# Kernel tuning notes

Measured on AMD Instinct MI355X. Metric: run time of the kernel, lower is better.

## Reference

```python
import jax, jax.numpy as jnp
import numpy as np

N, D, H = 100000, 128, 128
NB, NA, NP, NI = 120000, 200000, 250000, 30000


def _mlp(x, w1, b1, w2, b2):
    # small 2-layer readout MLP: Linear -> ReLU -> Linear
    return jnp.maximum(x @ w1 + b1, 0.0) @ w2 + b2


def _symmetry_pool(node_reps, idx, perms, w1, b1, w2, b2):
    # gather node reps by interaction indices, concat per permutation,
    # apply readout MLP, sum over symmetry permutations
    out = None
    for perm in perms:
        rep = jnp.concatenate([node_reps[idx[:, i]] for i in perm], axis=1)
        y = _mlp(rep, w1, b1, w2, b2)
        out = y if out is None else out + y
    return out


def setup_inputs() -> dict:
    key = jax.random.key(0)
    ks = jax.random.split(key, 32)
    inp = {
        'node_reps': jax.random.normal(ks[0], (N, D), dtype=jnp.float32),
        'bond_idx': jax.random.randint(ks[1], (NB, 2), 0, N),
        'angle_idx': jax.random.randint(ks[2], (NA, 3), 0, N),
        'proper_idx': jax.random.randint(ks[3], (NP, 4), 0, N),
        'improper_idx': jax.random.randint(ks[4], (NI, 4), 0, N),
    }
    # readout MLP params: (in_dim, out_dim) per term
    dims = {'a': (D, 2), 'b': (2 * D, 2), 'g': (3 * D, 2), 'p': (4 * D, 6), 'i': (4 * D, 6)}
    ki = 5
    for tag, (din, dout) in dims.items():
        inp[f'{tag}w1'] = jax.random.normal(ks[ki], (din, H), dtype=jnp.float32) * 0.05
        inp[f'{tag}b1'] = jnp.zeros((H,), dtype=jnp.float32)
        inp[f'{tag}w2'] = jax.random.normal(ks[ki + 1], (H, dout), dtype=jnp.float32) * 0.05
        inp[f'{tag}b2'] = jnp.zeros((dout,), dtype=jnp.float32)
        ki += 2
    return inp


def reference(node_reps, bond_idx, angle_idx, proper_idx, improper_idx,
              aw1, ab1, aw2, ab2,
              bw1, bb1, bw2, bb2,
              gw1, gb1, gw2, gb2,
              pw1, pb1, pw2, pb2,
              iw1, ib1, iw2, ib2):
    atoms = _mlp(node_reps, aw1, ab1, aw2, ab2)
    bonds = _symmetry_pool(node_reps, bond_idx, [(0, 1), (1, 0)], bw1, bb1, bw2, bb2)
    angles = _symmetry_pool(node_reps, angle_idx, [(0, 1, 2), (2, 1, 0)], gw1, gb1, gw2, gb2)
    propers = _symmetry_pool(node_reps, proper_idx, [(0, 1, 2, 3), (3, 2, 1, 0)], pw1, pb1, pw2, pb2)
    # improper perms: central atom at position 1, cyclic perms of others [0,2,3]
    improper_perms = [(0, 1, 2, 3), (2, 1, 3, 0), (3, 1, 0, 2)]
    impropers = _symmetry_pool(node_reps, improper_idx, improper_perms, iw1, ib1, iw2, ib2)
    return (atoms, bonds, angles, propers, impropers)
```

## Files before the change

### kernel.cpp

```cpp
#include <hip/hip_runtime.h>

#define PBLK 256

typedef __attribute__((ext_vector_type(8))) short bf16x8;
typedef __attribute__((ext_vector_type(16))) float f32x16;

__device__ __forceinline__ unsigned short f2bf(float x) {
    unsigned int u = __builtin_bit_cast(unsigned int, x);
    u += 0x7fffu + ((u >> 16) & 1u);
    return (unsigned short)(u >> 16);
}

__global__ void conv_node(const float* __restrict__ x, unsigned short* __restrict__ o, int n4) {
    int tid = blockIdx.x * PBLK + threadIdx.x;
    if (tid >= n4) return;
    const float4 v = reinterpret_cast<const float4*>(x)[tid];
    ushort4 r;
    r.x = f2bf(v.x); r.y = f2bf(v.y); r.z = f2bf(v.z); r.w = f2bf(v.w);
    reinterpret_cast<ushort4*>(o)[tid] = r;
}

template<int K>
__global__ void pack_w1(const float* __restrict__ w1, unsigned short* __restrict__ o) {
    constexpr int KS = K / 16;
    int tid = blockIdx.x * PBLK + threadIdx.x;
    if (tid >= K * 128) return;
    const int j = tid & 7;
    const int l = (tid >> 3) & 63;
    const int cts = tid >> 9;
    const int s  = cts % KS;
    const int ct = cts / KS;
    const int col = ct * 32 + (l & 31);
    const int k = s * 16 + (l >> 5) * 8 + j;
    o[tid] = f2bf(w1[(size_t)k * 128 + col]);
}

__global__ void pack_w2_all(const float* __restrict__ wa, const float* __restrict__ wb,
                            const float* __restrict__ wg, const float* __restrict__ wp,
                            const float* __restrict__ wi,
                            unsigned short* __restrict__ oa, unsigned short* __restrict__ ob,
                            unsigned short* __restrict__ og, unsigned short* __restrict__ op,
                            unsigned short* __restrict__ oi) {
    int tid = blockIdx.x * PBLK + threadIdx.x;
    if (tid >= 5 * 4096) return;
    const int term = tid >> 12, e = tid & 4095;
    const float* w; unsigned short* o; int dout;
    switch (term) {
        case 0: w = wa; o = oa; dout = 2; break;
        case 1: w = wb; o = ob; dout = 2; break;
        case 2: w = wg; o = og; dout = 2; break;
        case 3: w = wp; o = op; dout = 6; break;
        default: w = wi; o = oi; dout = 6; break;
    }
    const int j = e & 7, l = (e >> 3) & 63, s = e >> 9;
    const int col = l & 31;
    const int k = s * 16 + (l >> 5) * 8 + j;
    o[e] = (col < dout) ? f2bf(w[k * dout + col]) : (unsigned short)0;
}

__device__ __forceinline__ void gld_lds16(const unsigned short* g, unsigned char* l) {
    typedef __attribute__((address_space(1))) unsigned int GU;
    typedef __attribute__((address_space(3))) unsigned int LU;
    __builtin_amdgcn_global_load_lds((GU*)g, (LU*)l, 16, 0, 0);
}

template<int OFF>
__device__ __forceinline__ void glb16(bf16x8& d, const unsigned short* p) {
    if constexpr (OFF == 0)
        asm volatile("global_load_dwordx4 %0, %1, off" : "=v"(d) : "v"(p));
    else
        asm volatile("global_load_dwordx4 %0, %1, off offset:%2" : "=v"(d) : "v"(p), "i"(OFF));
}

template<int N> __device__ __forceinline__ void waitvm() {
    if constexpr (N == 0)       asm volatile("s_waitcnt vmcnt(0)"  ::: "memory");
    else if constexpr (N == 1)  asm volatile("s_waitcnt vmcnt(1)"  ::: "memory");
    else if constexpr (N == 2)  asm volatile("s_waitcnt vmcnt(2)"  ::: "memory");
    else if constexpr (N == 3)  asm volatile("s_waitcnt vmcnt(3)"  ::: "memory");
    else if constexpr (N == 4)  asm volatile("s_waitcnt vmcnt(4)"  ::: "memory");
    else if constexpr (N == 5)  asm volatile("s_waitcnt vmcnt(5)"  ::: "memory");
    else if constexpr (N == 6)  asm volatile("s_waitcnt vmcnt(6)"  ::: "memory");
    else if constexpr (N == 7)  asm volatile("s_waitcnt vmcnt(7)"  ::: "memory");
    else if constexpr (N == 8)  asm volatile("s_waitcnt vmcnt(8)"  ::: "memory");
    else if constexpr (N == 9)  asm volatile("s_waitcnt vmcnt(9)"  ::: "memory");
    else if constexpr (N == 10) asm volatile("s_waitcnt vmcnt(10)" ::: "memory");
    else if constexpr (N == 11) asm volatile("s_waitcnt vmcnt(11)" ::: "memory");
    else if constexpr (N == 12) asm volatile("s_waitcnt vmcnt(12)" ::: "memory");
    else                        asm volatile("s_waitcnt vmcnt(0)"  ::: "memory");
}

template<int TERM> struct TC;
template<> struct TC<0> { static constexpr int NA = 1, NP = 1, DO = 2;
                          static constexpr int P[1][4] = {{0,0,0,0}}; };
template<> struct TC<1> { static constexpr int NA = 2, NP = 2, DO = 2;
                          static constexpr int P[2][4] = {{0,1,0,0},{1,0,0,0}}; };
template<> struct TC<2> { static constexpr int NA = 3, NP = 2, DO = 2;
                          static constexpr int P[2][4] = {{0,1,2,0},{2,1,0,0}}; };
template<> struct TC<3> { static constexpr int NA = 4, NP = 2, DO = 6;
                          static constexpr int P[2][4] = {{0,1,2,3},{3,2,1,0}}; };
template<> struct TC<4> { static constexpr int NA = 4, NP = 3, DO = 6;
                          static constexpr int P[3][4] = {{0,1,2,3},{2,1,3,0},{3,1,0,2}}; };

template<int TERM>
__global__ __launch_bounds__(256, 2) void term_mfma(
    const unsigned short* __restrict__ nodeb,
    const int* __restrict__ idx,
    const unsigned short* __restrict__ pack,
    const unsigned short* __restrict__ pk2,
    const float* __restrict__ b1,
    const float* __restrict__ b2,
    float* __restrict__ out,
    int nrows, int ntiles)
{
    constexpr int NA   = TC<TERM>::NA;
    constexpr int NP   = TC<TERM>::NP;
    constexpr int DOUT = TC<TERM>::DO;
    constexpr int BUF  = NA * 8192;
    __shared__ __align__(16) unsigned char lds[2 * BUF];

    const int t    = threadIdx.x;
    const int l    = t & 63;
    const int w    = t >> 6;
    const int l31  = l & 31;
    const int hi   = l >> 5;
    const int l15  = l & 15;
    const int qr   = l >> 4;
    const int rowb = l31;
    const int GS   = gridDim.x;

    const unsigned short* pbp[NA][2];
    #pragma unroll
    for (int b = 0; b < NA; ++b)
        #pragma unroll
        for (int h = 0; h < 2; ++h)
            pbp[b][h] = pack + (((size_t)w * (NA * 8) + b * 8 + h * 4) * 64 + l) * 8;

    const int col = w * 32 + l31;
    const float bv = b1[col];
    const float b2v = (l31 < DOUT) ? b2[l31] * (float)NP : 0.0f;

    int nrw[NA * 2];
    int tile = blockIdx.x;

    #pragma unroll
    for (int a = 0; a < NA; ++a)
        #pragma unroll
        for (int q = 0; q < 2; ++q) {
            const int rl = w * 8 + q * 4 + qr;
            int gr = tile * 32 + rl; if (gr >= nrows) gr = nrows - 1;
            nrw[a * 2 + q] = idx ? idx[gr * NA + a] : gr;
        }
    #pragma unroll
    for (int a = 0; a < NA; ++a)
        #pragma unroll
        for (int q = 0; q < 2; ++q) {
            const int rl = w * 8 + q * 4 + qr;
            gld_lds16(nodeb + (size_t)nrw[a * 2 + q] * 128 + ((l15 ^ (rl & 15)) << 3),
                      lds + a * 8192 + (w * 8 + q * 4) * 256);
        }
    waitvm<0>();
    __builtin_amdgcn_s_barrier();

    int cur = 0;
    for (; tile < ntiles; tile += GS) {
        const bool hasnext = (tile + GS) < ntiles;
        unsigned char* xb = lds + cur * BUF;
        unsigned char* ob = lds + (cur ^ 1) * BUF;

        if (hasnext) {
            #pragma unroll
            for (int a = 0; a < NA; ++a)
                #pragma unroll
                for (int q = 0; q < 2; ++q) {
                    const int rl = w * 8 + q * 4 + qr;
                    int gr = (tile + GS) * 32 + rl; if (gr >= nrows) gr = nrows - 1;
                    nrw[a * 2 + q] = idx ? idx[gr * NA + a] : gr;
                }
        }

        f32x16 acc[NP];
        #pragma unroll
        for (int p = 0; p < NP; ++p)
            #pragma unroll
            for (int i = 0; i < 16; ++i) acc[p][i] = bv;

        bf16x8 Bf[4][NA];
#define ISSUEB(J) do { _Pragma("unroll")                                           \
        for (int b = 0; b < NA; ++b)                                               \
            glb16<((J) & 3) * 1024>(Bf[(J) & 3][b], pbp[b][(J) >> 2]); } while (0)

        ISSUEB(0); ISSUEB(1); ISSUEB(2); ISSUEB(3);

#define KSTEP(C) do {                                                              \
        waitvm<NA * (((7 - (C)) < 3) ? (7 - (C)) : 3)>();                          \
        __builtin_amdgcn_sched_barrier(0);                                         \
        bf16x8 av[NA];                                                             \
        _Pragma("unroll")                                                          \
        for (int s = 0; s < NA; ++s)                                               \
            av[s] = *reinterpret_cast<const bf16x8*>(                              \
                xb + s * 8192 + rowb * 256 + ((((C) * 2 + hi) ^ (rowb & 15)) << 4)); \
        _Pragma("unroll")                                                          \
        for (int b = 0; b < NA; ++b) {                                             \
            _Pragma("unroll")                                                      \
            for (int p = 0; p < NP; ++p)                                           \
                acc[p] = __builtin_amdgcn_mfma_f32_32x32x16_bf16(                  \
                    av[TC<TERM>::P[p][b]], Bf[(C) & 3][b], acc[p], 0, 0, 0);       \
        }                                                                          \
        if constexpr ((C) + 4 <= 7) ISSUEB((C) + 4);                               \
    } while (0)

        KSTEP(0); KSTEP(1); KSTEP(2); KSTEP(3);
        KSTEP(4); KSTEP(5); KSTEP(6); KSTEP(7);
#undef KSTEP
#undef ISSUEB

        __builtin_amdgcn_s_barrier();

        if (hasnext) {
            #pragma unroll
            for (int a = 0; a < NA; ++a)
                #pragma unroll
                for (int q = 0; q < 2; ++q) {
                    const int rl = w * 8 + q * 4 + qr;
                    gld_lds16(nodeb + (size_t)nrw[a * 2 + q] * 128 + ((l15 ^ (rl & 15)) << 3),
                              ob + a * 8192 + (w * 8 + q * 4) * 256);
                }
        }

        #pragma unroll
        for (int i = 0; i < 16; ++i) {
            const int rowl = (i & 3) + 8 * (i >> 2) + 4 * hi;
            float v = 0.0f;
            #pragma unroll
            for (int p = 0; p < NP; ++p) v += fmaxf(acc[p][i], 0.0f);
            *reinterpret_cast<unsigned short*>(
                xb + rowl * 256 + (((col >> 3) ^ (rowl & 15)) << 4) + (col & 7) * 2) = f2bf(v);
        }
        asm volatile("s_waitcnt lgkmcnt(0)" ::: "memory");
        __builtin_amdgcn_s_barrier();

        {
            f32x16 a2;
            #pragma unroll
            for (int i = 0; i < 16; ++i) a2[i] = 0.0f;
            #pragma unroll
            for (int s = 0; s < 8; ++s) {
                const bf16x8 ah = *reinterpret_cast<const bf16x8*>(
                    xb + rowb * 256 + (((s * 2 + hi) ^ (rowb & 15)) << 4));
                const bf16x8 bw = *reinterpret_cast<const bf16x8*>(pk2 + ((size_t)s * 64 + l) * 8);
                a2 = __builtin_amdgcn_mfma_f32_32x32x16_bf16(ah, bw, a2, 0, 0, 0);
            }
            if (w == 0 && l31 < DOUT) {
                #pragma unroll
                for (int i = 0; i < 16; ++i) {
                    const int rowl = (i & 3) + 8 * (i >> 2) + 4 * hi;
                    const int grow = tile * 32 + rowl;
                    if (grow < nrows) out[(size_t)grow * DOUT + l31] = a2[i] + b2v;
                }
            }
        }
        __builtin_amdgcn_sched_barrier(0);
        waitvm<0>();
        __builtin_amdgcn_s_barrier();
        cur ^= 1;
    }
}

extern "C" void kernel_launch(void* const* d_in, const int* in_sizes, int n_in,
                              void* d_out, int out_size, void* d_ws, size_t ws_size,
                              hipStream_t stream) {
    const float* node = (const float*)d_in[0];
    const int* bidx = (const int*)d_in[1];
    const int* gidx = (const int*)d_in[2];
    const int* pidx = (const int*)d_in[3];
    const int* iidx = (const int*)d_in[4];

    const float* aw1 = (const float*)d_in[5];
    const float* ab1 = (const float*)d_in[6];
    const float* aw2 = (const float*)d_in[7];
    const float* ab2 = (const float*)d_in[8];
    const float* bw1 = (const float*)d_in[9];
    const float* bb1 = (const float*)d_in[10];
    const float* bw2 = (const float*)d_in[11];
    const float* bb2 = (const float*)d_in[12];
    const float* gw1 = (const float*)d_in[13];
    const float* gb1 = (const float*)d_in[14];
    const float* gw2 = (const float*)d_in[15];
    const float* gb2 = (const float*)d_in[16];
    const float* pw1 = (const float*)d_in[17];
    const float* pb1 = (const float*)d_in[18];
    const float* pw2 = (const float*)d_in[19];
    const float* pb2 = (const float*)d_in[20];
    const float* iw1 = (const float*)d_in[21];
    const float* ib1 = (const float*)d_in[22];
    const float* iw2 = (const float*)d_in[23];
    const float* ib2 = (const float*)d_in[24];

    const int N   = in_sizes[0] / 128;
    const int NB  = in_sizes[1] / 2;
    const int NAg = in_sizes[2] / 3;
    const int NP_ = in_sizes[3] / 4;
    const int NI  = in_sizes[4] / 4;

    float* out   = (float*)d_out;
    float* out_a = out;
    float* out_b = out_a + (size_t)N   * 2;
    float* out_g = out_b + (size_t)NB  * 2;
    float* out_p = out_g + (size_t)NAg * 2;
    float* out_i = out_p + (size_t)NP_ * 6;

    unsigned short* nodeb = (unsigned short*)d_ws;
    size_t off = (size_t)N * 128;
    unsigned short* packA = nodeb + off; off += (size_t)128 * 128;
    unsigned short* packB = nodeb + off; off += (size_t)256 * 128;
    unsigned short* packG = nodeb + off; off += (size_t)384 * 128;
    unsigned short* packP = nodeb + off; off += (size_t)512 * 128;
    unsigned short* packI = nodeb + off; off += (size_t)512 * 128;
    unsigned short* pk2A  = nodeb + off; off += 4096;
    unsigned short* pk2B  = nodeb + off; off += 4096;
    unsigned short* pk2G  = nodeb + off; off += 4096;
    unsigned short* pk2P  = nodeb + off; off += 4096;
    unsigned short* pk2I  = nodeb + off; off += 4096;

    {
        const int n4 = N * 128 / 4;
        conv_node<<<(n4 + PBLK - 1) / PBLK, PBLK, 0, stream>>>(node, nodeb, n4);
    }
    pack_w1<128><<<(128 * 128 + PBLK - 1) / PBLK, PBLK, 0, stream>>>(aw1, packA);
    pack_w1<256><<<(256 * 128 + PBLK - 1) / PBLK, PBLK, 0, stream>>>(bw1, packB);
    pack_w1<384><<<(384 * 128 + PBLK - 1) / PBLK, PBLK, 0, stream>>>(gw1, packG);
    pack_w1<512><<<(512 * 128 + PBLK - 1) / PBLK, PBLK, 0, stream>>>(pw1, packP);
    pack_w1<512><<<(512 * 128 + PBLK - 1) / PBLK, PBLK, 0, stream>>>(iw1, packI);
    pack_w2_all<<<(5 * 4096 + PBLK - 1) / PBLK, PBLK, 0, stream>>>(
        aw2, bw2, gw2, pw2, iw2, pk2A, pk2B, pk2G, pk2P, pk2I);

    const int nt0 = (N   + 31) / 32, g0 = nt0 < 1024 ? nt0 : 1024;
    const int nt1 = (NB  + 31) / 32, g1 = nt1 < 1024 ? nt1 : 1024;
    const int nt2 = (NAg + 31) / 32, g2 = nt2 <  768 ? nt2 :  768;
    const int nt3 = (NP_ + 31) / 32, g3 = nt3 <  512 ? nt3 :  512;
    const int nt4 = (NI  + 31) / 32, g4 = nt4 <  512 ? nt4 :  512;

    term_mfma<0><<<g0, 256, 0, stream>>>(nodeb, nullptr, packA, pk2A, ab1, ab2, out_a, N,   nt0);
    term_mfma<1><<<g1, 256, 0, stream>>>(nodeb, bidx,    packB, pk2B, bb1, bb2, out_b, NB,  nt1);
    term_mfma<2><<<g2, 256, 0, stream>>>(nodeb, gidx,    packG, pk2G, gb1, gb2, out_g, NAg, nt2);
    term_mfma<3><<<g3, 256, 0, stream>>>(nodeb, pidx,    packP, pk2P, pb1, pb2, out_p, NP_, nt3);
    term_mfma<4><<<g4, 256, 0, stream>>>(nodeb, iidx,    packI, pk2I, ib1, ib2, out_i, NI,  nt4);
}
```

Before: 257.9 us.

## Single-buffer gathered node tiles in LDS and raise occupancy per term

Replaces the double-buffered LDS tile with a single buffer so each block needs half the shared memory. Prefetch of the next tile's gathered rows is moved to after the first-layer MFMAs, and the last atom slot, reused as the hidden-activation scratch, is reloaded only after the second layer finishes. Launch bounds now allow more waves per CU for each term, and grid caps for angles and propers are raised to match. The cost is less overlap between gather latency and compute, plus an extra barrier per tile, in exchange for more resident blocks to hide latency.

After: 372.8 us. +44.5%, slower.

```diff
diff --git a/kernel.cpp b/kernel.cpp
--- a/kernel.cpp
+++ b/kernel.cpp
@@ -78,13 +78,9 @@
     else if constexpr (N == 2)  asm volatile("s_waitcnt vmcnt(2)"  ::: "memory");
     else if constexpr (N == 3)  asm volatile("s_waitcnt vmcnt(3)"  ::: "memory");
     else if constexpr (N == 4)  asm volatile("s_waitcnt vmcnt(4)"  ::: "memory");
-    else if constexpr (N == 5)  asm volatile("s_waitcnt vmcnt(5)"  ::: "memory");
     else if constexpr (N == 6)  asm volatile("s_waitcnt vmcnt(6)"  ::: "memory");
-    else if constexpr (N == 7)  asm volatile("s_waitcnt vmcnt(7)"  ::: "memory");
     else if constexpr (N == 8)  asm volatile("s_waitcnt vmcnt(8)"  ::: "memory");
     else if constexpr (N == 9)  asm volatile("s_waitcnt vmcnt(9)"  ::: "memory");
-    else if constexpr (N == 10) asm volatile("s_waitcnt vmcnt(10)" ::: "memory");
-    else if constexpr (N == 11) asm volatile("s_waitcnt vmcnt(11)" ::: "memory");
     else if constexpr (N == 12) asm volatile("s_waitcnt vmcnt(12)" ::: "memory");
     else                        asm volatile("s_waitcnt vmcnt(0)"  ::: "memory");
 }
@@ -101,8 +97,8 @@
 template<> struct TC<4> { static constexpr int NA = 4, NP = 3, DO = 6;
                           static constexpr int P[3][4] = {{0,1,2,3},{2,1,3,0},{3,1,0,2}}; };
 
-template<int TERM>
-__global__ __launch_bounds__(256, 2) void term_mfma(
+template<int TERM, int MINW>
+__global__ __launch_bounds__(256, MINW) void term_mfma(
     const unsigned short* __restrict__ nodeb,
     const int* __restrict__ idx,
     const unsigned short* __restrict__ pack,
@@ -116,7 +112,7 @@
     constexpr int NP   = TC<TERM>::NP;
     constexpr int DOUT = TC<TERM>::DO;
     constexpr int BUF  = NA * 8192;
-    __shared__ __align__(16) unsigned char lds[2 * BUF];
+    __shared__ __align__(16) unsigned char lds[BUF];
 
     const int t    = threadIdx.x;
     const int l    = t & 63;
@@ -127,6 +123,7 @@
     const int qr   = l >> 4;
     const int rowb = l31;
     const int GS   = gridDim.x;
+    unsigned char* hb = lds + (NA - 1) * 8192;
 
     const unsigned short* pbp[NA][2];
     #pragma unroll
@@ -161,11 +158,8 @@
     waitvm<0>();
     __builtin_amdgcn_s_barrier();
 
-    int cur = 0;
     for (; tile < ntiles; tile += GS) {
         const bool hasnext = (tile + GS) < ntiles;
-        unsigned char* xb = lds + cur * BUF;
-        unsigned char* ob = lds + (cur ^ 1) * BUF;
 
         if (hasnext) {
             #pragma unroll
@@ -188,9 +182,6 @@
 #define ISSUEB(J) do { _Pragma("unroll")                                           \
         for (int b = 0; b < NA; ++b)                                               \
             glb16<((J) & 3) * 1024>(Bf[(J) & 3][b], pbp[b][(J) >> 2]); } while (0)
-
-        ISSUEB(0); ISSUEB(1); ISSUEB(2); ISSUEB(3);
-
 #define KSTEP(C) do {                                                              \
         waitvm<NA * (((7 - (C)) < 3) ? (7 - (C)) : 3)>();                          \
         __builtin_amdgcn_sched_barrier(0);                                         \
@@ -198,7 +189,7 @@
         _Pragma("unroll")                                                          \
         for (int s = 0; s < NA; ++s)                                               \
             av[s] = *reinterpret_cast<const bf16x8*>(                              \
-                xb + s * 8192 + rowb * 256 + ((((C) * 2 + hi) ^ (rowb & 15)) << 4)); \
+                lds + s * 8192 + rowb * 256 + ((((C) * 2 + hi) ^ (rowb & 15)) << 4)); \
         _Pragma("unroll")                                                          \
         for (int b = 0; b < NA; ++b) {                                             \
             _Pragma("unroll")                                                      \
@@ -208,7 +199,7 @@
         }                                                                          \
         if constexpr ((C) + 4 <= 7) ISSUEB((C) + 4);                               \
     } while (0)
-
+        ISSUEB(0); ISSUEB(1); ISSUEB(2); ISSUEB(3);
         KSTEP(0); KSTEP(1); KSTEP(2); KSTEP(3);
         KSTEP(4); KSTEP(5); KSTEP(6); KSTEP(7);
 #undef KSTEP
@@ -218,12 +209,12 @@
 
         if (hasnext) {
             #pragma unroll
-            for (int a = 0; a < NA; ++a)
+            for (int a = 0; a < NA - 1; ++a)
                 #pragma unroll
                 for (int q = 0; q < 2; ++q) {
                     const int rl = w * 8 + q * 4 + qr;
                     gld_lds16(nodeb + (size_t)nrw[a * 2 + q] * 128 + ((l15 ^ (rl & 15)) << 3),
-                              ob + a * 8192 + (w * 8 + q * 4) * 256);
+                              lds + a * 8192 + (w * 8 + q * 4) * 256);
                 }
         }
 
@@ -234,7 +225,7 @@
             #pragma unroll
             for (int p = 0; p < NP; ++p) v += fmaxf(acc[p][i], 0.0f);
             *reinterpret_cast<unsigned short*>(
-                xb + rowl * 256 + (((col >> 3) ^ (rowl & 15)) << 4) + (col & 7) * 2) = f2bf(v);
+                hb + rowl * 256 + (((col >> 3) ^ (rowl & 15)) << 4) + (col & 7) * 2) = f2bf(v);
         }
         asm volatile("s_waitcnt lgkmcnt(0)" ::: "memory");
         __builtin_amdgcn_s_barrier();
@@ -246,7 +237,7 @@
             #pragma unroll
             for (int s = 0; s < 8; ++s) {
                 const bf16x8 ah = *reinterpret_cast<const bf16x8*>(
-                    xb + rowb * 256 + (((s * 2 + hi) ^ (rowb & 15)) << 4));
+                    hb + rowb * 256 + (((s * 2 + hi) ^ (rowb & 15)) << 4));
                 const bf16x8 bw = *reinterpret_cast<const bf16x8*>(pk2 + ((size_t)s * 64 + l) * 8);
                 a2 = __builtin_amdgcn_mfma_f32_32x32x16_bf16(ah, bw, a2, 0, 0, 0);
             }
@@ -259,10 +250,20 @@
                 }
             }
         }
+        asm volatile("s_waitcnt lgkmcnt(0)" ::: "memory");
+        __builtin_amdgcn_s_barrier();
+
+        if (hasnext) {
+            #pragma unroll
+            for (int q = 0; q < 2; ++q) {
+                const int rl = w * 8 + q * 4 + qr;
+                gld_lds16(nodeb + (size_t)nrw[(NA - 1) * 2 + q] * 128 + ((l15 ^ (rl & 15)) << 3),
+                          lds + (NA - 1) * 8192 + (w * 8 + q * 4) * 256);
+            }
+        }
         __builtin_amdgcn_sched_barrier(0);
         waitvm<0>();
         __builtin_amdgcn_s_barrier();
-        cur ^= 1;
     }
 }
 
@@ -336,13 +337,13 @@
 
     const int nt0 = (N   + 31) / 32, g0 = nt0 < 1024 ? nt0 : 1024;
     const int nt1 = (NB  + 31) / 32, g1 = nt1 < 1024 ? nt1 : 1024;
-    const int nt2 = (NAg + 31) / 32, g2 = nt2 <  768 ? nt2 :  768;
-    const int nt3 = (NP_ + 31) / 32, g3 = nt3 <  512 ? nt3 :  512;
+    const int nt2 = (NAg + 31) / 32, g2 = nt2 < 1024 ? nt2 : 1024;
+    const int nt3 = (NP_ + 31) / 32, g3 = nt3 <  768 ? nt3 :  768;
     const int nt4 = (NI  + 31) / 32, g4 = nt4 <  512 ? nt4 :  512;
 
-    term_mfma<0><<<g0, 256, 0, stream>>>(nodeb, nullptr, packA, pk2A, ab1, ab2, out_a, N,   nt0);
-    term_mfma<1><<<g1, 256, 0, stream>>>(nodeb, bidx,    packB, pk2B, bb1, bb2, out_b, NB,  nt1);
-    term_mfma<2><<<g2, 256, 0, stream>>>(nodeb, gidx,    packG, pk2G, gb1, gb2, out_g, NAg, nt2);
-    term_mfma<3><<<g3, 256, 0, stream>>>(nodeb, pidx,    packP, pk2P, pb1, pb2, out_p, NP_, nt3);
-    term_mfma<4><<<g4, 256, 0, stream>>>(nodeb, iidx,    packI, pk2I, ib1, ib2, out_i, NI,  nt4);
-}
+    term_mfma<0, 4><<<g0, 256, 0, stream>>>(nodeb, nullptr, packA, pk2A, ab1, ab2, out_a, N,   nt0);
+    term_mfma<1, 4><<<g1, 256, 0, stream>>>(nodeb, bidx,    packB, pk2B, bb1, bb2, out_b, NB,  nt1);
+    term_mfma<2, 4><<<g2, 256, 0, stream>>>(nodeb, gidx,    packG, pk2G, gb1, gb2, out_g, NAg, nt2);
+    term_mfma<3, 3><<<g3, 256, 0, stream>>>(nodeb, pidx,    packP, pk2P, pb1, pb2, out_p, NP_, nt3);
+    term_mfma<4, 2><<<g4, 256, 0, stream>>>(nodeb, iidx,    packI, pk2I, ib1, ib2, out_i, NI,  nt4);
+}
```

## Fuse five term kernels into one launch with work-proportional block split

Applied to the files above, without the earlier changes.

Replaces the five sequential per-term MFMA kernel launches with one fused kernel. Block ranges are dispatched to each term's body, with the persistent grid sized per term roughly in proportion to its work (512 blocks total). All terms then run concurrently instead of serially, which removes launch gaps and per-kernel tail effects. The risk is that the fixed LDS allocation (64KB, sized for the 4-atom terms) cuts occupancy for the small terms, and that a poorly balanced split leaves a tail where the proper-torsion blocks finish last.

After: 292.9 us. 1.14x slower.

```diff
diff --git a/kernel.cpp b/kernel.cpp
--- a/kernel.cpp
+++ b/kernel.cpp
@@ -78,13 +78,9 @@
     else if constexpr (N == 2)  asm volatile("s_waitcnt vmcnt(2)"  ::: "memory");
     else if constexpr (N == 3)  asm volatile("s_waitcnt vmcnt(3)"  ::: "memory");
     else if constexpr (N == 4)  asm volatile("s_waitcnt vmcnt(4)"  ::: "memory");
-    else if constexpr (N == 5)  asm volatile("s_waitcnt vmcnt(5)"  ::: "memory");
     else if constexpr (N == 6)  asm volatile("s_waitcnt vmcnt(6)"  ::: "memory");
-    else if constexpr (N == 7)  asm volatile("s_waitcnt vmcnt(7)"  ::: "memory");
     else if constexpr (N == 8)  asm volatile("s_waitcnt vmcnt(8)"  ::: "memory");
     else if constexpr (N == 9)  asm volatile("s_waitcnt vmcnt(9)"  ::: "memory");
-    else if constexpr (N == 10) asm volatile("s_waitcnt vmcnt(10)" ::: "memory");
-    else if constexpr (N == 11) asm volatile("s_waitcnt vmcnt(11)" ::: "memory");
     else if constexpr (N == 12) asm volatile("s_waitcnt vmcnt(12)" ::: "memory");
     else                        asm volatile("s_waitcnt vmcnt(0)"  ::: "memory");
 }
@@ -102,7 +98,8 @@
                           static constexpr int P[3][4] = {{0,1,2,3},{2,1,3,0},{3,1,0,2}}; };
 
 template<int TERM>
-__global__ __launch_bounds__(256, 2) void term_mfma(
+__device__ __forceinline__ void term_body(
+    unsigned char* lds,
     const unsigned short* __restrict__ nodeb,
     const int* __restrict__ idx,
     const unsigned short* __restrict__ pack,
@@ -110,13 +107,12 @@
     const float* __restrict__ b1,
     const float* __restrict__ b2,
     float* __restrict__ out,
-    int nrows, int ntiles)
+    int nrows, int ntiles, int bid0, int GS)
 {
     constexpr int NA   = TC<TERM>::NA;
     constexpr int NP   = TC<TERM>::NP;
     constexpr int DOUT = TC<TERM>::DO;
     constexpr int BUF  = NA * 8192;
-    __shared__ __align__(16) unsigned char lds[2 * BUF];
 
     const int t    = threadIdx.x;
     const int l    = t & 63;
@@ -126,7 +122,6 @@
     const int l15  = l & 15;
     const int qr   = l >> 4;
     const int rowb = l31;
-    const int GS   = gridDim.x;
 
     const unsigned short* pbp[NA][2];
     #pragma unroll
@@ -140,7 +135,7 @@
     const float b2v = (l31 < DOUT) ? b2[l31] * (float)NP : 0.0f;
 
     int nrw[NA * 2];
-    int tile = blockIdx.x;
+    int tile = bid0;
 
     #pragma unroll
     for (int a = 0; a < NA; ++a)
@@ -164,8 +159,8 @@
     int cur = 0;
     for (; tile < ntiles; tile += GS) {
         const bool hasnext = (tile + GS) < ntiles;
-        unsigned char* xb = lds + cur * BUF;
-        unsigned char* ob = lds + (cur ^ 1) * BUF;
+        unsigned char* xb   = lds + cur * BUF;
+        unsigned char* obuf = lds + (cur ^ 1) * BUF;
 
         if (hasnext) {
             #pragma unroll
@@ -188,9 +183,6 @@
 #define ISSUEB(J) do { _Pragma("unroll")                                           \
         for (int b = 0; b < NA; ++b)                                               \
             glb16<((J) & 3) * 1024>(Bf[(J) & 3][b], pbp[b][(J) >> 2]); } while (0)
-
-        ISSUEB(0); ISSUEB(1); ISSUEB(2); ISSUEB(3);
-
 #define KSTEP(C) do {                                                              \
         waitvm<NA * (((7 - (C)) < 3) ? (7 - (C)) : 3)>();                          \
         __builtin_amdgcn_sched_barrier(0);                                         \
@@ -209,6 +201,7 @@
         if constexpr ((C) + 4 <= 7) ISSUEB((C) + 4);                               \
     } while (0)
 
+        ISSUEB(0); ISSUEB(1); ISSUEB(2); ISSUEB(3);
         KSTEP(0); KSTEP(1); KSTEP(2); KSTEP(3);
         KSTEP(4); KSTEP(5); KSTEP(6); KSTEP(7);
 #undef KSTEP
@@ -223,7 +216,7 @@
                 for (int q = 0; q < 2; ++q) {
                     const int rl = w * 8 + q * 4 + qr;
                     gld_lds16(nodeb + (size_t)nrw[a * 2 + q] * 128 + ((l15 ^ (rl & 15)) << 3),
-                              ob + a * 8192 + (w * 8 + q * 4) * 256);
+                              obuf + a * 8192 + (w * 8 + q * 4) * 256);
                 }
         }
 
@@ -264,6 +257,44 @@
         __builtin_amdgcn_s_barrier();
         cur ^= 1;
     }
+}
+
+struct FArgs {
+    const unsigned short* nodeb;
+    const int *bidx, *gidx, *pidx, *iidx;
+    const unsigned short *packA, *packB, *packG, *packP, *packI;
+    const unsigned short *pk2A, *pk2B, *pk2G, *pk2P, *pk2I;
+    const float *ab1, *ab2, *bb1, *bb2, *gb1, *gb2, *pb1, *pb2, *ib1, *ib2;
+    float *oa, *ob, *og, *op, *oi;
+    int N, NB, NG, NP_, NI;
+    int ntA, ntB, ntG, ntP, ntI;
+    int gA, gB, gG, gP, gI;
+};
+
+__global__ __launch_bounds__(256, 2) void fused_terms(FArgs a) {
+    __shared__ __align__(16) unsigned char lds[65536];
+    int b = blockIdx.x;
+    if (b < a.gA) {
+        term_body<0>(lds, a.nodeb, nullptr, a.packA, a.pk2A, a.ab1, a.ab2, a.oa, a.N,   a.ntA, b, a.gA);
+        return;
+    }
+    b -= a.gA;
+    if (b < a.gB) {
+        term_body<1>(lds, a.nodeb, a.bidx,  a.packB, a.pk2B, a.bb1, a.bb2, a.ob, a.NB,  a.ntB, b, a.gB);
+        return;
+    }
+    b -= a.gB;
+    if (b < a.gG) {
+        term_body<2>(lds, a.nodeb, a.gidx,  a.packG, a.pk2G, a.gb1, a.gb2, a.og, a.NG,  a.ntG, b, a.gG);
+        return;
+    }
+    b -= a.gG;
+    if (b < a.gP) {
+        term_body<3>(lds, a.nodeb, a.pidx,  a.packP, a.pk2P, a.pb1, a.pb2, a.op, a.NP_, a.ntP, b, a.gP);
+        return;
+    }
+    b -= a.gP;
+    term_body<4>(lds, a.nodeb, a.iidx,  a.packI, a.pk2I, a.ib1, a.ib2, a.oi, a.NI,  a.ntI, b, a.gI);
 }
 
 extern "C" void kernel_launch(void* const* d_in, const int* in_sizes, int n_in,
@@ -298,7 +329,7 @@
 
     const int N   = in_sizes[0] / 128;
     const int NB  = in_sizes[1] / 2;
-    const int NAg = in_sizes[2] / 3;
+    const int NG  = in_sizes[2] / 3;
     const int NP_ = in_sizes[3] / 4;
     const int NI  = in_sizes[4] / 4;
 
@@ -306,7 +337,7 @@
     float* out_a = out;
     float* out_b = out_a + (size_t)N   * 2;
     float* out_g = out_b + (size_t)NB  * 2;
-    float* out_p = out_g + (size_t)NAg * 2;
+    float* out_p = out_g + (size_t)NG  * 2;
     float* out_i = out_p + (size_t)NP_ * 6;
 
     unsigned short* nodeb = (unsigned short*)d_ws;
@@ -334,15 +365,26 @@
     pack_w2_all<<<(5 * 4096 + PBLK - 1) / PBLK, PBLK, 0, stream>>>(
         aw2, bw2, gw2, pw2, iw2, pk2A, pk2B, pk2G, pk2P, pk2I);
 
-    const int nt0 = (N   + 31) / 32, g0 = nt0 < 1024 ? nt0 : 1024;
-    const int nt1 = (NB  + 31) / 32, g1 = nt1 < 1024 ? nt1 : 1024;
-    const int nt2 = (NAg + 31) / 32, g2 = nt2 <  768 ? nt2 :  768;
-    const int nt3 = (NP_ + 31) / 32, g3 = nt3 <  512 ? nt3 :  512;
-    const int nt4 = (NI  + 31) / 32, g4 = nt4 <  512 ? nt4 :  512;
-
-    term_mfma<0><<<g0, 256, 0, stream>>>(nodeb, nullptr, packA, pk2A, ab1, ab2, out_a, N,   nt0);
-    term_mfma<1><<<g1, 256, 0, stream>>>(nodeb, bidx,    packB, pk2B, bb1, bb2, out_b, NB,  nt1);
-    term_mfma<2><<<g2, 256, 0, stream>>>(nodeb, gidx,    packG, pk2G, gb1, gb2, out_g, NAg, nt2);
-    term_mfma<3><<<g3, 256, 0, stream>>>(nodeb, pidx,    packP, pk2P, pb1, pb2, out_p, NP_, nt3);
-    term_mfma<4><<<g4, 256, 0, stream>>>(nodeb, iidx,    packI, pk2I, ib1, ib2, out_i, NI,  nt4);
-}
+    FArgs a;
+    a.nodeb = nodeb;
+    a.bidx = bidx; a.gidx = gidx; a.pidx = pidx; a.iidx = iidx;
+    a.packA = packA; a.packB = packB; a.packG = packG; a.packP = packP; a.packI = packI;
+    a.pk2A = pk2A; a.pk2B = pk2B; a.pk2G = pk2G; a.pk2P = pk2P; a.pk2I = pk2I;
+    a.ab1 = ab1; a.ab2 = ab2; a.bb1 = bb1; a.bb2 = bb2;
+    a.gb1 = gb1; a.gb2 = gb2; a.pb1 = pb1; a.pb2 = pb2; a.ib1 = ib1; a.ib2 = ib2;
+    a.oa = out_a; a.ob = out_b; a.og = out_g; a.op = out_p; a.oi = out_i;
+    a.N = N; a.NB = NB; a.NG = NG; a.NP_ = NP_; a.NI = NI;
+    a.ntA = (N   + 31) / 32;
+    a.ntB = (NB  + 31) / 32;
+    a.ntG = (NG  + 31) / 32;
+    a.ntP = (NP_ + 31) / 32;
+    a.ntI = (NI  + 31) / 32;
+    a.gA = a.ntA < 28  ? a.ntA : 28;
+    a.gB = a.ntB < 68  ? a.ntB : 68;
+    a.gG = a.ntG < 148 ? a.ntG : 148;
+    a.gP = a.ntP < 228 ? a.ntP : 228;
+    a.gI = a.ntI < 40  ? a.ntI : 40;
+    const int grid = a.gA + a.gB + a.gG + a.gP + a.gI;
+
+    fused_terms<<<grid, 256, 0, stream>>>(a);
+}
```
